# Performance work log

Hardware: AMD Instinct MI355X
Metric: run time of the kernel (lower is better)

Reference implementation:

```python
import jax, jax.numpy as jnp
import numpy as np

B, C, H, W = 2, 64, 128, 128
HEADS = 8
HID = C  # hidden_size = dim in MHSA.__init__
EPS = 1e-12  # F.normalize default eps


def setup_inputs() -> dict:
    key = jax.random.key(0)
    ks = jax.random.split(key, 9)
    s = 0.05
    return {
        "x": jax.random.normal(ks[0], (B, C, H, W), jnp.float32),
        "W1": jax.random.normal(ks[1], (C, HID), jnp.float32) * s,
        "b1": jax.random.normal(ks[2], (C, HID), jnp.float32) * s,
        "W2": jax.random.normal(ks[3], (C, HID, HID), jnp.float32) * s,
        "b2": jax.random.normal(ks[4], (C, HID), jnp.float32) * s,
        "W3": jax.random.normal(ks[5], (C, HID, 3), jnp.float32) * s,
        "b3": jax.random.normal(ks[6], (C, 3), jnp.float32) * s,
        "temperature": jnp.ones((HEADS, 1, 1), jnp.float32),
        "Wout": jax.random.normal(ks[7], (C, C), jnp.float32) * s,  # [out, in] 1x1 conv
        "bout": jax.random.normal(ks[8], (C,), jnp.float32) * s,
    }


def reference(x, W1, b1, W2, b2, W3, b3, temperature, Wout, bout):
    b, c, h, w = x.shape
    # KAN QKV projection: per-channel tiny MLPs, batched over the channel axis.
    xt = jnp.transpose(x, (0, 2, 3, 1)).reshape(-1, c)          # [N, C]
    h1 = jax.nn.relu(xt[:, :, None] * W1[None] + b1[None])      # [N, C, HID]
    h2 = jax.nn.relu(jnp.einsum('nch,chk->nck', h1, W2) + b2[None])  # [N, C, HID]
    o = jnp.einsum('nch,cho->nco', h2, W3) + b3[None]           # [N, C, 3]
    # torch.cat of per-channel 3-col outputs along dim=1 == reshape [N, C*3]
    qkv = o.reshape(b, h, w, c * 3)
    qkv = jnp.transpose(qkv, (0, 3, 1, 2))                      # [b, 3c, h, w]
    q, k, v = jnp.split(qkv, 3, axis=1)                         # each [b, c, h, w]

    def to_heads(t):
        return t.reshape(b, HEADS, c // HEADS, h * w)

    q, k, v = to_heads(q), to_heads(k), to_heads(v)
    # L2-normalize along the spatial (last) axis, torch F.normalize semantics
    q = q / jnp.maximum(jnp.linalg.norm(q, axis=-1, keepdims=True), EPS)
    k = k / jnp.maximum(jnp.linalg.norm(k, axis=-1, keepdims=True), EPS)
    # Channel attention: [b, head, c_h, c_h]
    attn = jnp.einsum('bhcn,bhdn->bhcd', q, k) * temperature[None]
    attn = jax.nn.softmax(attn, axis=-1)
    out = jnp.einsum('bhcd,bhdn->bhcn', attn, v)                # [b, head, c_h, hw]
    out = out.reshape(b, c, h, w)
    # 1x1 conv projection
    out = jnp.einsum('bchw,oc->bohw', out, Wout) + bout[None, :, None, None]
    return out
```

## Files before the change

### kernel.cpp

```cpp
#include <hip/hip_runtime.h>
#include <hip/hip_bf16.h>
#include <math.h>

#define HW 16384
#define NCH 64

#define NG   2048
#define X0   (-8.0f)
#define INVDX 128.0f
#define DX   0.0078125f
#define PSTR (64*2048)

typedef __attribute__((ext_vector_type(8))) short s16x8;
typedef __attribute__((ext_vector_type(4))) short s16x4;
typedef __attribute__((ext_vector_type(2))) float f32x2;
typedef __attribute__((ext_vector_type(4))) float f32x4;
typedef __attribute__((ext_vector_type(8))) float f32x8;
typedef __attribute__((ext_vector_type(2))) __bf16 bf16x2;
typedef __attribute__((ext_vector_type(8))) __bf16 bf16x8;
typedef __attribute__((ext_vector_type(4))) unsigned u32x4;
typedef __attribute__((ext_vector_type(2))) unsigned u32x2;

__device__ __forceinline__ short bf16b(float f) {
    union { __hip_bfloat16 h; short s; } u;
    u.h = __float2bfloat16(f);
    return u.s;
}
__device__ __forceinline__ float bf2f(unsigned short us) {
    union { unsigned u; float f; } x;
    x.u = ((unsigned)us) << 16;
    return x.f;
}
__device__ __forceinline__ s16x8 cvt8(f32x8 v) {
    return __builtin_bit_cast(s16x8, __builtin_convertvector(v, bf16x8));
}
__device__ __forceinline__ unsigned pk_h1(f32x2 xw, f32x2 w, f32x2 b, f32x2 z2) {
    const f32x2 h = __builtin_elementwise_max(__builtin_elementwise_fma(xw, w, b), z2);
    return __builtin_bit_cast(unsigned, __builtin_convertvector(h, bf16x2));
}
__device__ __forceinline__ unsigned pk_relu_cvt(f32x2 v, f32x2 z2) {
    const f32x2 g = __builtin_elementwise_max(v, z2);
    return __builtin_bit_cast(unsigned, __builtin_convertvector(g, bf16x2));
}

#if __has_builtin(__builtin_amdgcn_mfma_f32_16x16x16bf16_1k)
#define HAVE_MFMA16 1
#else
#define HAVE_MFMA16 0
#endif

__global__ __launch_bounds__(64, 4) void kan_grid_mfma(
    const float* __restrict__ W1,
    const float* __restrict__ b1,
    const float* __restrict__ W2,
    const float* __restrict__ b2,
    const float* __restrict__ W3,
    const float* __restrict__ b3,
    float* __restrict__ table)
{
    const int c     = blockIdx.x & 63;
    const int chunk = blockIdx.x >> 6;
    const int lane  = threadIdx.x;
    const int l15   = lane & 15;
    const int grp   = lane >> 4;

    __shared__ float W2s[4096];
    __shared__ float W1s[64], B1s[64], B2s[64];
    {
        const float4* src = (const float4*)(W2 + c * 4096);
        float4* dst = (float4*)W2s;
        for (int i = lane; i < 1024; i += 64) dst[i] = src[i];
        W1s[lane] = W1[c*64 + lane];
        B1s[lane] = b1[c*64 + lane];
        B2s[lane] = b2[c*64 + lane];
    }
    __syncthreads();

    const float* W3c = W3 + c * 192;

    s16x8 a1[4][2];
#pragma unroll
    for (int m = 0; m < 4; ++m)
#pragma unroll
        for (int s = 0; s < 2; ++s) {
            f32x8 w;
#pragma unroll
            for (int jj = 0; jj < 8; ++jj)
                w[jj] = W2s[(s*32 + grp*8 + jj)*64 + m*16 + l15];
            a1[m][s] = cvt8(w);
        }

#if HAVE_MFMA16
    s16x4 a2[4];
#pragma unroll
    for (int m = 0; m < 4; ++m) {
        s16x4 f;
#pragma unroll
        for (int jj = 0; jj < 4; ++jj) {
            const int k = m*16 + grp*4 + jj;
            f[jj] = (l15 < 3) ? bf16b(W3c[k*3 + l15]) : (short)0;
        }
        a2[m] = f;
    }
    f32x4 b3r;
#pragma unroll
    for (int r = 0; r < 4; ++r) {
        const int row = grp*4 + r;
        b3r[r] = (row < 3) ? b3[c*3 + row] : 0.f;
    }
#else
    const float b3v0 = b3[c*3+0], b3v1 = b3[c*3+1], b3v2 = b3[c*3+2];
#endif

    float* Tq = table + c*NG;
    const char* b2base = (const char*)B2s;
    const f32x2 z2 = {0.f, 0.f};

    for (int t = 0; t < 16; ++t) {
        int z;
        asm volatile("v_mov_b32 %0, 0" : "=v"(z));

        const int pt = chunk*256 + t*16 + l15;
        const float xv = X0 + (float)pt * DX;
        const f32x2 xw = {xv, xv};

        s16x8 bf[2];
#pragma unroll
        for (int s = 0; s < 2; ++s) {
            const f32x4 w1lo = *(const f32x4*)&W1s[z + s*32 + grp*8];
            const f32x4 w1hi = *(const f32x4*)&W1s[z + s*32 + grp*8 + 4];
            const f32x4 b1lo = *(const f32x4*)&B1s[z + s*32 + grp*8];
            const f32x4 b1hi = *(const f32x4*)&B1s[z + s*32 + grp*8 + 4];
            u32x4 p;
            p[0] = pk_h1(xw, (f32x2){w1lo[0], w1lo[1]}, (f32x2){b1lo[0], b1lo[1]}, z2);
            p[1] = pk_h1(xw, (f32x2){w1lo[2], w1lo[3]}, (f32x2){b1lo[2], b1lo[3]}, z2);
            p[2] = pk_h1(xw, (f32x2){w1hi[0], w1hi[1]}, (f32x2){b1hi[0], b1hi[1]}, z2);
            p[3] = pk_h1(xw, (f32x2){w1hi[2], w1hi[3]}, (f32x2){b1hi[2], b1hi[3]}, z2);
            bf[s] = __builtin_bit_cast(s16x8, p);
        }

        f32x4 acc[4];
#pragma unroll
        for (int m = 0; m < 4; ++m) {
            acc[m] = *(const f32x4*)(b2base + (m*64 + grp*16 + z));
            acc[m] = __builtin_amdgcn_mfma_f32_16x16x32_bf16(a1[m][0], bf[0], acc[m], 0, 0, 0);
            acc[m] = __builtin_amdgcn_mfma_f32_16x16x32_bf16(a1[m][1], bf[1], acc[m], 0, 0, 0);
        }

#if HAVE_MFMA16
        s16x4 bb[4];
#pragma unroll
        for (int m = 0; m < 4; ++m) {
            u32x2 pv;
            pv[0] = pk_relu_cvt((f32x2){acc[m][0], acc[m][1]}, z2);
            pv[1] = pk_relu_cvt((f32x2){acc[m][2], acc[m][3]}, z2);
            bb[m] = __builtin_bit_cast(s16x4, pv);
        }
        f32x4 acc2a = b3r;
        f32x4 acc2b = {0.f, 0.f, 0.f, 0.f};
        acc2a = __builtin_amdgcn_mfma_f32_16x16x16bf16_1k(a2[0], bb[0], acc2a, 0, 0, 0);
        acc2b = __builtin_amdgcn_mfma_f32_16x16x16bf16_1k(a2[1], bb[1], acc2b, 0, 0, 0);
        acc2a = __builtin_amdgcn_mfma_f32_16x16x16bf16_1k(a2[2], bb[2], acc2a, 0, 0, 0);
        acc2b = __builtin_amdgcn_mfma_f32_16x16x16bf16_1k(a2[3], bb[3], acc2b, 0, 0, 0);
        if (grp == 0) {
            Tq[pt]          = acc2a[0] + acc2b[0];
            Tq[PSTR + pt]   = acc2a[1] + acc2b[1];
            Tq[2*PSTR + pt] = acc2a[2] + acc2b[2];
        }
#else
        float po0 = 0.f, po1 = 0.f, po2 = 0.f;
#pragma unroll
        for (int m = 0; m < 4; ++m)
#pragma unroll
            for (int r = 0; r < 4; ++r) {
                const float g = fmaxf(acc[m][r], 0.f);
                const int k = m*16 + grp*4 + r;
                po0 = fmaf(g, W3c[k*3+0], po0);
                po1 = fmaf(g, W3c[k*3+1], po1);
                po2 = fmaf(g, W3c[k*3+2], po2);
            }
        po0 += __shfl_xor(po0, 16, 64); po0 += __shfl_xor(po0, 32, 64);
        po1 += __shfl_xor(po1, 16, 64); po1 += __shfl_xor(po1, 32, 64);
        po2 += __shfl_xor(po2, 16, 64); po2 += __shfl_xor(po2, 32, 64);
        if (grp == 0) {
            Tq[pt]          = po0 + b3v0;
            Tq[PSTR + pt]   = po1 + b3v1;
            Tq[2*PSTR + pt] = po2 + b3v2;
        }
#endif
    }
}

__global__ __launch_bounds__(512) void gram_kernel(
    const float* __restrict__ x, const float* __restrict__ table,
    float* __restrict__ dpart)
{
    const int bhd = blockIdx.x >> 4;
    const int spl = blockIdx.x & 15;
    const int b = bhd >> 3, hd = bhd & 7;
    const int tid = threadIdx.x;
    const int w   = tid >> 6;
    const int l   = tid & 63;
    const int grp = l >> 4;
    const int i16 = l & 15;
    const int ch  = i16 & 7;
    const int usek = i16 >> 3;

    __shared__ unsigned short T[2][8][NG];

    for (int e = tid; e < 8192; e += 512) {
        const int map = e >> 12;
        const int rem = e & 4095;
        const int c8  = rem >> 9;
        const int g   = rem & 511;
        const int gm  = map*64 + hd*8 + c8;
        const int cc  = gm / 3;
        const int jj  = gm % 3;
        const float4 v = ((const float4*)(table + jj*PSTR + cc*NG))[g];
        u32x2 pk;
        pk[0] = ((unsigned)(unsigned short)bf16b(v.x)) | (((unsigned)(unsigned short)bf16b(v.y)) << 16);
        pk[1] = ((unsigned)(unsigned short)bf16b(v.z)) | (((unsigned)(unsigned short)bf16b(v.w)) << 16);
        *(u32x2*)&T[map][c8][g*4] = pk;
    }
    __syncthreads();

    const unsigned short* Tc = T[usek][ch];
    const int gm = usek*64 + hd*8 + ch;
    const int cx = gm / 3;
    const float* xp = x + (b*NCH + cx)*HW + spl*1024 + grp*8;

    f32x4 gacc = {0.f, 0.f, 0.f, 0.f};
#pragma unroll
    for (int s = 0; s < 4; ++s) {
        const int slab = w*4 + s;
        const float* xs = xp + slab*32;
        const f32x4 xlo = *(const f32x4*)xs;
        const f32x4 xhi = *(const f32x4*)(xs + 4);
        f32x8 vals;
#pragma unroll
        for (int e = 0; e < 8; ++e) {
            const float xv = (e < 4) ? xlo[e] : xhi[e-4];
            const float u = (xv - X0) * INVDX;
            int idx = (int)u;
            idx = min(max(idx, 0), NG - 2);
            const float fr = u - (float)idx;
            const float t0 = bf2f(Tc[idx]);
            const float t1 = bf2f(Tc[idx+1]);
            vals[e] = fmaf(fr, t1 - t0, t0);
        }
        const s16x8 frag = cvt8(vals);
        gacc = __builtin_amdgcn_mfma_f32_16x16x32_bf16(frag, frag, gacc, 0, 0, 0);
    }

    __syncthreads();
    float* red = (float*)&T[0][0][0];
#pragma unroll
    for (int r = 0; r < 4; ++r)
        red[w*256 + (grp*4 + r)*16 + i16] = gacc[r];
    __syncthreads();

    if (tid < 256) {
        const int row = tid >> 4, col = tid & 15;
        float g = 0.f;
#pragma unroll
        for (int ww = 0; ww < 8; ++ww) g += red[ww*256 + tid];
        int p = -1;
        if (row < 8 && col >= 8)      p = row*8 + (col - 8);
        else if (row == col && row < 8) p = 64 + row;
        else if (row == col)            p = 72 + (row - 8);
        if (p >= 0) dpart[(bhd*16 + spl)*80 + p] = g;
    }
}

__global__ __launch_bounds__(256) void v_eval(
    const float* __restrict__ x, const float* __restrict__ table,
    unsigned short* __restrict__ vbuf)
{
    const int m     = blockIdx.x >> 3;
    const int chunk = blockIdx.x & 7;
    const int t     = threadIdx.x;
    const int gm    = 128 + m;
    const int cx    = gm / 3;
    const int jj    = gm % 3;

    __shared__ float Lv[NG];
    const float4* Tv = (const float4*)(table + jj*PSTR + cx*NG);
    for (int i = t; i < NG/4; i += 256) ((float4*)Lv)[i] = Tv[i];
    __syncthreads();

    const int pxbase = chunk * 4096;
    const int b  = pxbase >> 14;
    const int hw = pxbase & 16383;
    const float* xr = x + (b*NCH + cx)*HW + hw;
    unsigned short* vr = vbuf + (b*NCH + m)*HW + hw;

    for (int i = 0; i < 8; ++i) {
        const int off = i*512 + t*2;
        const float2 xv = *(const float2*)(xr + off);
        float o[2];
#pragma unroll
        for (int e = 0; e < 2; ++e) {
            const float u = ((e ? xv.y : xv.x) - X0) * INVDX;
            int idx = (int)u;
            idx = min(max(idx, 0), NG - 2);
            const float fr = u - (float)idx;
            const float v0 = Lv[idx], v1 = Lv[idx+1];
            o[e] = fmaf(fr, v1 - v0, v0);
        }
        ushort2 vs;
        vs.x = (unsigned short)bf16b(o[0]);
        vs.y = (unsigned short)bf16b(o[1]);
        *(ushort2*)(vr + off) = vs;
    }
}

__global__ __launch_bounds__(256) void out_kernel(
    const unsigned short* __restrict__ vbuf, const float* __restrict__ dpart,
    const float* __restrict__ temp, const float* __restrict__ Wout,
    const float* __restrict__ bout, float* __restrict__ out)
{
    const int b    = blockIdx.x >> 8;
    const int qtr  = (blockIdx.x >> 6) & 3;
    const int tile = blockIdx.x & 63;
    const int n = tile * 256 + threadIdx.x;
    const int t = threadIdx.x;

    __shared__ float D[8][80];
    __shared__ float attnS[8][8][8];
    __shared__ float4 AtS[64][4];

    for (int idx = t; idx < 640; idx += 256) {
        const int g = idx / 80, p = idx % 80;
        float s = 0.f;
        for (int spl = 0; spl < 16; ++spl)
            s += dpart[((b*8 + g)*16 + spl)*80 + p];
        D[g][p] = s;
    }
    __syncthreads();

    if (t < 64) {
        const int hd = t >> 3, i = t & 7;
        const float invq = 1.f / fmaxf(sqrtf(D[hd][64+i]), 1e-12f);
        const float T = temp[hd];
        float l[8];
        float m = -1e30f;
#pragma unroll
        for (int j = 0; j < 8; ++j) {
            const float invk = 1.f / fmaxf(sqrtf(D[hd][72+j]), 1e-12f);
            l[j] = D[hd][i*8+j] * invq * invk * T;
            m = fmaxf(m, l[j]);
        }
        float s = 0.f;
#pragma unroll
        for (int j = 0; j < 8; ++j) { l[j] = expf(l[j] - m); s += l[j]; }
        const float inv = 1.f / s;
#pragma unroll
        for (int j = 0; j < 8; ++j) attnS[hd][i][j] = l[j] * inv;
    }
    __syncthreads();

    {
        const int cv = t & 63, oq = t >> 6;
        const int hd = cv >> 3, jj = cv & 7;
        float res[4];
#pragma unroll
        for (int oo = 0; oo < 4; ++oo) {
            const int o = qtr*16 + oq*4 + oo;
            float s = 0.f;
#pragma unroll
            for (int i = 0; i < 8; ++i)
                s = fmaf(Wout[o*64 + hd*8 + i], attnS[hd][i][jj], s);
            res[oo] = s;
        }
        AtS[cv][oq] = make_float4(res[0], res[1], res[2], res[3]);
    }
    __syncthreads();

    float acc[16];
#pragma unroll
    for (int o = 0; o < 16; ++o) acc[o] = 0.f;

    const unsigned short* vbase = vbuf + (b*NCH)*HW + n;
    for (int cv = 0; cv < 64; ++cv) {
        const float vv = bf2f(vbase[cv*HW]);
#pragma unroll
        for (int o4 = 0; o4 < 4; ++o4) {
            const float4 w = AtS[cv][o4];
            acc[4*o4+0] = fmaf(w.x, vv, acc[4*o4+0]);
            acc[4*o4+1] = fmaf(w.y, vv, acc[4*o4+1]);
            acc[4*o4+2] = fmaf(w.z, vv, acc[4*o4+2]);
            acc[4*o4+3] = fmaf(w.w, vv, acc[4*o4+3]);
        }
    }
#pragma unroll
    for (int o = 0; o < 16; ++o) {
        const int oc = qtr*16 + o;
        out[(b*NCH + oc)*HW + n] = acc[o] + bout[oc];
    }
}

extern "C" void kernel_launch(void* const* d_in, const int* in_sizes, int n_in,
                              void* d_out, int out_size, void* d_ws, size_t ws_size,
                              hipStream_t stream) {
    const float* x    = (const float*)d_in[0];
    const float* W1   = (const float*)d_in[1];
    const float* b1   = (const float*)d_in[2];
    const float* W2   = (const float*)d_in[3];
    const float* b2   = (const float*)d_in[4];
    const float* W3   = (const float*)d_in[5];
    const float* b3   = (const float*)d_in[6];
    const float* temp = (const float*)d_in[7];
    const float* Wout = (const float*)d_in[8];
    const float* bout = (const float*)d_in[9];
    float* out = (float*)d_out;

    float* ws = (float*)d_ws;
    float* table = ws;
    float* dpart = ws + 393216;
    unsigned short* vbuf = (unsigned short*)(ws + 393216 + 20480);

    kan_grid_mfma<<<512, 64, 0, stream>>>(W1, b1, W2, b2, W3, b3, table);
    gram_kernel<<<256, 512, 0, stream>>>(x, table, dpart);
    v_eval<<<512, 256, 0, stream>>>(x, table, vbuf);
    out_kernel<<<512, 256, 0, stream>>>(vbuf, dpart, temp, Wout, bout, out);
}
```

Baseline: 52.78 us.

## Fuse four kernels into one cooperative kernel with grid-wide syncs

Merges the table-build, gram, v-eval and output kernels into a single cooperative launch of 256 blocks of 512 threads, separated by grid.sync(). The work split per block changes: the table phase runs on only 64 blocks, and v-eval and output cover larger slices per block. The aim is to remove three kernel-launch gaps and inter-kernel drain/fill. In exchange, grid syncs add their own cost, and the table phase leaves most of the grid idle with larger per-block work.

```diff
diff --git a/kernel.cpp b/kernel.cpp
--- a/kernel.cpp
+++ b/kernel.cpp
@@ -1,6 +1,9 @@
 #include <hip/hip_runtime.h>
+#include <hip/hip_cooperative_groups.h>
 #include <hip/hip_bf16.h>
 #include <math.h>
+
+namespace cg = cooperative_groups;
 
 #define HW 16384
 #define NCH 64
@@ -49,353 +52,356 @@
 #define HAVE_MFMA16 0
 #endif
 
-__global__ __launch_bounds__(64, 4) void kan_grid_mfma(
-    const float* __restrict__ W1,
-    const float* __restrict__ b1,
-    const float* __restrict__ W2,
-    const float* __restrict__ b2,
-    const float* __restrict__ W3,
-    const float* __restrict__ b3,
-    float* __restrict__ table)
-{
-    const int c     = blockIdx.x & 63;
-    const int chunk = blockIdx.x >> 6;
-    const int lane  = threadIdx.x;
-    const int l15   = lane & 15;
-    const int grp   = lane >> 4;
-
-    __shared__ float W2s[4096];
-    __shared__ float W1s[64], B1s[64], B2s[64];
-    {
-        const float4* src = (const float4*)(W2 + c * 4096);
-        float4* dst = (float4*)W2s;
-        for (int i = lane; i < 1024; i += 64) dst[i] = src[i];
-        W1s[lane] = W1[c*64 + lane];
-        B1s[lane] = b1[c*64 + lane];
-        B2s[lane] = b2[c*64 + lane];
-    }
-    __syncthreads();
-
-    const float* W3c = W3 + c * 192;
-
-    s16x8 a1[4][2];
-#pragma unroll
-    for (int m = 0; m < 4; ++m)
-#pragma unroll
-        for (int s = 0; s < 2; ++s) {
-            f32x8 w;
-#pragma unroll
-            for (int jj = 0; jj < 8; ++jj)
-                w[jj] = W2s[(s*32 + grp*8 + jj)*64 + m*16 + l15];
-            a1[m][s] = cvt8(w);
-        }
-
-#if HAVE_MFMA16
-    s16x4 a2[4];
-#pragma unroll
-    for (int m = 0; m < 4; ++m) {
-        s16x4 f;
-#pragma unroll
-        for (int jj = 0; jj < 4; ++jj) {
-            const int k = m*16 + grp*4 + jj;
-            f[jj] = (l15 < 3) ? bf16b(W3c[k*3 + l15]) : (short)0;
-        }
-        a2[m] = f;
-    }
-    f32x4 b3r;
-#pragma unroll
-    for (int r = 0; r < 4; ++r) {
-        const int row = grp*4 + r;
-        b3r[r] = (row < 3) ? b3[c*3 + row] : 0.f;
-    }
-#else
-    const float b3v0 = b3[c*3+0], b3v1 = b3[c*3+1], b3v2 = b3[c*3+2];
-#endif
-
-    float* Tq = table + c*NG;
-    const char* b2base = (const char*)B2s;
-    const f32x2 z2 = {0.f, 0.f};
-
-    for (int t = 0; t < 16; ++t) {
-        int z;
-        asm volatile("v_mov_b32 %0, 0" : "=v"(z));
-
-        const int pt = chunk*256 + t*16 + l15;
-        const float xv = X0 + (float)pt * DX;
-        const f32x2 xw = {xv, xv};
-
-        s16x8 bf[2];
-#pragma unroll
-        for (int s = 0; s < 2; ++s) {
-            const f32x4 w1lo = *(const f32x4*)&W1s[z + s*32 + grp*8];
-            const f32x4 w1hi = *(const f32x4*)&W1s[z + s*32 + grp*8 + 4];
-            const f32x4 b1lo = *(const f32x4*)&B1s[z + s*32 + grp*8];
-            const f32x4 b1hi = *(const f32x4*)&B1s[z + s*32 + grp*8 + 4];
-            u32x4 p;
-            p[0] = pk_h1(xw, (f32x2){w1lo[0], w1lo[1]}, (f32x2){b1lo[0], b1lo[1]}, z2);
-            p[1] = pk_h1(xw, (f32x2){w1lo[2], w1lo[3]}, (f32x2){b1lo[2], b1lo[3]}, z2);
-            p[2] = pk_h1(xw, (f32x2){w1hi[0], w1hi[1]}, (f32x2){b1hi[0], b1hi[1]}, z2);
-            p[3] = pk_h1(xw, (f32x2){w1hi[2], w1hi[3]}, (f32x2){b1hi[2], b1hi[3]}, z2);
-            bf[s] = __builtin_bit_cast(s16x8, p);
-        }
-
-        f32x4 acc[4];
-#pragma unroll
-        for (int m = 0; m < 4; ++m) {
-            acc[m] = *(const f32x4*)(b2base + (m*64 + grp*16 + z));
-            acc[m] = __builtin_amdgcn_mfma_f32_16x16x32_bf16(a1[m][0], bf[0], acc[m], 0, 0, 0);
-            acc[m] = __builtin_amdgcn_mfma_f32_16x16x32_bf16(a1[m][1], bf[1], acc[m], 0, 0, 0);
-        }
-
-#if HAVE_MFMA16
-        s16x4 bb[4];
-#pragma unroll
-        for (int m = 0; m < 4; ++m) {
-            u32x2 pv;
-            pv[0] = pk_relu_cvt((f32x2){acc[m][0], acc[m][1]}, z2);
-            pv[1] = pk_relu_cvt((f32x2){acc[m][2], acc[m][3]}, z2);
-            bb[m] = __builtin_bit_cast(s16x4, pv);
-        }
-        f32x4 acc2a = b3r;
-        f32x4 acc2b = {0.f, 0.f, 0.f, 0.f};
-        acc2a = __builtin_amdgcn_mfma_f32_16x16x16bf16_1k(a2[0], bb[0], acc2a, 0, 0, 0);
-        acc2b = __builtin_amdgcn_mfma_f32_16x16x16bf16_1k(a2[1], bb[1], acc2b, 0, 0, 0);
-        acc2a = __builtin_amdgcn_mfma_f32_16x16x16bf16_1k(a2[2], bb[2], acc2a, 0, 0, 0);
-        acc2b = __builtin_amdgcn_mfma_f32_16x16x16bf16_1k(a2[3], bb[3], acc2b, 0, 0, 0);
-        if (grp == 0) {
-            Tq[pt]          = acc2a[0] + acc2b[0];
-            Tq[PSTR + pt]   = acc2a[1] + acc2b[1];
-            Tq[2*PSTR + pt] = acc2a[2] + acc2b[2];
-        }
-#else
-        float po0 = 0.f, po1 = 0.f, po2 = 0.f;
-#pragma unroll
-        for (int m = 0; m < 4; ++m)
-#pragma unroll
-            for (int r = 0; r < 4; ++r) {
-                const float g = fmaxf(acc[m][r], 0.f);
-                const int k = m*16 + grp*4 + r;
-                po0 = fmaf(g, W3c[k*3+0], po0);
-                po1 = fmaf(g, W3c[k*3+1], po1);
-                po2 = fmaf(g, W3c[k*3+2], po2);
-            }
-        po0 += __shfl_xor(po0, 16, 64); po0 += __shfl_xor(po0, 32, 64);
-        po1 += __shfl_xor(po1, 16, 64); po1 += __shfl_xor(po1, 32, 64);
-        po2 += __shfl_xor(po2, 16, 64); po2 += __shfl_xor(po2, 32, 64);
-        if (grp == 0) {
-            Tq[pt]          = po0 + b3v0;
-            Tq[PSTR + pt]   = po1 + b3v1;
-            Tq[2*PSTR + pt] = po2 + b3v2;
-        }
-#endif
-    }
-}
-
-__global__ __launch_bounds__(512) void gram_kernel(
-    const float* __restrict__ x, const float* __restrict__ table,
-    float* __restrict__ dpart)
-{
-    const int bhd = blockIdx.x >> 4;
-    const int spl = blockIdx.x & 15;
-    const int b = bhd >> 3, hd = bhd & 7;
-    const int tid = threadIdx.x;
-    const int w   = tid >> 6;
-    const int l   = tid & 63;
-    const int grp = l >> 4;
-    const int i16 = l & 15;
-    const int ch  = i16 & 7;
-    const int usek = i16 >> 3;
-
-    __shared__ unsigned short T[2][8][NG];
-
-    for (int e = tid; e < 8192; e += 512) {
-        const int map = e >> 12;
-        const int rem = e & 4095;
-        const int c8  = rem >> 9;
-        const int g   = rem & 511;
-        const int gm  = map*64 + hd*8 + c8;
-        const int cc  = gm / 3;
-        const int jj  = gm % 3;
-        const float4 v = ((const float4*)(table + jj*PSTR + cc*NG))[g];
-        u32x2 pk;
-        pk[0] = ((unsigned)(unsigned short)bf16b(v.x)) | (((unsigned)(unsigned short)bf16b(v.y)) << 16);
-        pk[1] = ((unsigned)(unsigned short)bf16b(v.z)) | (((unsigned)(unsigned short)bf16b(v.w)) << 16);
-        *(u32x2*)&T[map][c8][g*4] = pk;
-    }
-    __syncthreads();
-
-    const unsigned short* Tc = T[usek][ch];
-    const int gm = usek*64 + hd*8 + ch;
-    const int cx = gm / 3;
-    const float* xp = x + (b*NCH + cx)*HW + spl*1024 + grp*8;
-
-    f32x4 gacc = {0.f, 0.f, 0.f, 0.f};
-#pragma unroll
-    for (int s = 0; s < 4; ++s) {
-        const int slab = w*4 + s;
-        const float* xs = xp + slab*32;
-        const f32x4 xlo = *(const f32x4*)xs;
-        const f32x4 xhi = *(const f32x4*)(xs + 4);
-        f32x8 vals;
-#pragma unroll
-        for (int e = 0; e < 8; ++e) {
-            const float xv = (e < 4) ? xlo[e] : xhi[e-4];
-            const float u = (xv - X0) * INVDX;
-            int idx = (int)u;
-            idx = min(max(idx, 0), NG - 2);
-            const float fr = u - (float)idx;
-            const float t0 = bf2f(Tc[idx]);
-            const float t1 = bf2f(Tc[idx+1]);
-            vals[e] = fmaf(fr, t1 - t0, t0);
-        }
-        const s16x8 frag = cvt8(vals);
-        gacc = __builtin_amdgcn_mfma_f32_16x16x32_bf16(frag, frag, gacc, 0, 0, 0);
-    }
-
-    __syncthreads();
-    float* red = (float*)&T[0][0][0];
-#pragma unroll
-    for (int r = 0; r < 4; ++r)
-        red[w*256 + (grp*4 + r)*16 + i16] = gacc[r];
-    __syncthreads();
-
-    if (tid < 256) {
-        const int row = tid >> 4, col = tid & 15;
-        float g = 0.f;
-#pragma unroll
-        for (int ww = 0; ww < 8; ++ww) g += red[ww*256 + tid];
-        int p = -1;
-        if (row < 8 && col >= 8)      p = row*8 + (col - 8);
-        else if (row == col && row < 8) p = 64 + row;
-        else if (row == col)            p = 72 + (row - 8);
-        if (p >= 0) dpart[(bhd*16 + spl)*80 + p] = g;
-    }
-}
-
-__global__ __launch_bounds__(256) void v_eval(
-    const float* __restrict__ x, const float* __restrict__ table,
+__global__ __launch_bounds__(512, 2) void fused_mhsa(
+    const float* __restrict__ x,
+    const float* __restrict__ W1, const float* __restrict__ b1,
+    const float* __restrict__ W2, const float* __restrict__ b2,
+    const float* __restrict__ W3, const float* __restrict__ b3,
+    const float* __restrict__ temp, const float* __restrict__ Wout,
+    const float* __restrict__ bout, float* __restrict__ out,
+    float* __restrict__ table, float* __restrict__ dpart,
     unsigned short* __restrict__ vbuf)
 {
-    const int m     = blockIdx.x >> 3;
-    const int chunk = blockIdx.x & 7;
-    const int t     = threadIdx.x;
-    const int gm    = 128 + m;
-    const int cx    = gm / 3;
-    const int jj    = gm % 3;
-
-    __shared__ float Lv[NG];
-    const float4* Tv = (const float4*)(table + jj*PSTR + cx*NG);
-    for (int i = t; i < NG/4; i += 256) ((float4*)Lv)[i] = Tv[i];
-    __syncthreads();
-
-    const int pxbase = chunk * 4096;
-    const int b  = pxbase >> 14;
-    const int hw = pxbase & 16383;
-    const float* xr = x + (b*NCH + cx)*HW + hw;
-    unsigned short* vr = vbuf + (b*NCH + m)*HW + hw;
-
-    for (int i = 0; i < 8; ++i) {
-        const int off = i*512 + t*2;
-        const float2 xv = *(const float2*)(xr + off);
-        float o[2];
-#pragma unroll
-        for (int e = 0; e < 2; ++e) {
-            const float u = ((e ? xv.y : xv.x) - X0) * INVDX;
-            int idx = (int)u;
-            idx = min(max(idx, 0), NG - 2);
-            const float fr = u - (float)idx;
-            const float v0 = Lv[idx], v1 = Lv[idx+1];
-            o[e] = fmaf(fr, v1 - v0, v0);
-        }
-        ushort2 vs;
-        vs.x = (unsigned short)bf16b(o[0]);
-        vs.y = (unsigned short)bf16b(o[1]);
-        *(ushort2*)(vr + off) = vs;
+    __shared__ __align__(16) unsigned char LB[65536];
+    cg::grid_group grid = cg::this_grid();
+    const int bi  = blockIdx.x;
+    const int tid = threadIdx.x;
+
+    if (bi < 64) {
+        const int c = bi;
+        float* W2s = (float*)LB;
+        float* W1s = (float*)(LB + 16384);
+        float* B1s = (float*)(LB + 16640);
+        float* B2s = (float*)(LB + 16896);
+        {
+            const float4* src = (const float4*)(W2 + c * 4096);
+            float4* dst = (float4*)W2s;
+            for (int i = tid; i < 1024; i += 512) dst[i] = src[i];
+            if (tid < 64) {
+                W1s[tid] = W1[c*64 + tid];
+                B1s[tid] = b1[c*64 + tid];
+                B2s[tid] = b2[c*64 + tid];
+            }
+        }
+        __syncthreads();
+
+        const int lane  = tid & 63;
+        const int chunk = tid >> 6;
+        const int l15   = lane & 15;
+        const int grp   = lane >> 4;
+        const float* W3c = W3 + c * 192;
+
+        s16x8 a1[4][2];
+#pragma unroll
+        for (int m = 0; m < 4; ++m)
+#pragma unroll
+            for (int s = 0; s < 2; ++s) {
+                f32x8 w;
+#pragma unroll
+                for (int jj = 0; jj < 8; ++jj)
+                    w[jj] = W2s[(s*32 + grp*8 + jj)*64 + m*16 + l15];
+                a1[m][s] = cvt8(w);
+            }
+
+#if HAVE_MFMA16
+        s16x4 a2[4];
+#pragma unroll
+        for (int m = 0; m < 4; ++m) {
+            s16x4 f;
+#pragma unroll
+            for (int jj = 0; jj < 4; ++jj) {
+                const int k = m*16 + grp*4 + jj;
+                f[jj] = (l15 < 3) ? bf16b(W3c[k*3 + l15]) : (short)0;
+            }
+            a2[m] = f;
+        }
+        f32x4 b3r;
+#pragma unroll
+        for (int r = 0; r < 4; ++r) {
+            const int row = grp*4 + r;
+            b3r[r] = (row < 3) ? b3[c*3 + row] : 0.f;
+        }
+#else
+        const float b3v0 = b3[c*3+0], b3v1 = b3[c*3+1], b3v2 = b3[c*3+2];
+#endif
+
+        float* Tq = table + c*NG;
+        const char* b2base = (const char*)B2s;
+        const f32x2 z2 = {0.f, 0.f};
+
+        for (int t = 0; t < 16; ++t) {
+            int z;
+            asm volatile("v_mov_b32 %0, 0" : "=v"(z));
+
+            const int pt = chunk*256 + t*16 + l15;
+            const float xv = X0 + (float)pt * DX;
+            const f32x2 xw = {xv, xv};
+
+            s16x8 bf[2];
+#pragma unroll
+            for (int s = 0; s < 2; ++s) {
+                const f32x4 w1lo = *(const f32x4*)&W1s[z + s*32 + grp*8];
+                const f32x4 w1hi = *(const f32x4*)&W1s[z + s*32 + grp*8 + 4];
+                const f32x4 b1lo = *(const f32x4*)&B1s[z + s*32 + grp*8];
+                const f32x4 b1hi = *(const f32x4*)&B1s[z + s*32 + grp*8 + 4];
+                u32x4 p;
+                p[0] = pk_h1(xw, (f32x2){w1lo[0], w1lo[1]}, (f32x2){b1lo[0], b1lo[1]}, z2);
+                p[1] = pk_h1(xw, (f32x2){w1lo[2], w1lo[3]}, (f32x2){b1lo[2], b1lo[3]}, z2);
+                p[2] = pk_h1(xw, (f32x2){w1hi[0], w1hi[1]}, (f32x2){b1hi[0], b1hi[1]}, z2);
+                p[3] = pk_h1(xw, (f32x2){w1hi[2], w1hi[3]}, (f32x2){b1hi[2], b1hi[3]}, z2);
+                bf[s] = __builtin_bit_cast(s16x8, p);
+            }
+
+            f32x4 acc[4];
+#pragma unroll
+            for (int m = 0; m < 4; ++m) {
+                acc[m] = *(const f32x4*)(b2base + (m*64 + grp*16 + z));
+                acc[m] = __builtin_amdgcn_mfma_f32_16x16x32_bf16(a1[m][0], bf[0], acc[m], 0, 0, 0);
+                acc[m] = __builtin_amdgcn_mfma_f32_16x16x32_bf16(a1[m][1], bf[1], acc[m], 0, 0, 0);
+            }
+
+#if HAVE_MFMA16
+            s16x4 bb[4];
+#pragma unroll
+            for (int m = 0; m < 4; ++m) {
+                u32x2 pv;
+                pv[0] = pk_relu_cvt((f32x2){acc[m][0], acc[m][1]}, z2);
+                pv[1] = pk_relu_cvt((f32x2){acc[m][2], acc[m][3]}, z2);
+                bb[m] = __builtin_bit_cast(s16x4, pv);
+            }
+            f32x4 acc2a = b3r;
+            f32x4 acc2b = {0.f, 0.f, 0.f, 0.f};
+            acc2a = __builtin_amdgcn_mfma_f32_16x16x16bf16_1k(a2[0], bb[0], acc2a, 0, 0, 0);
+            acc2b = __builtin_amdgcn_mfma_f32_16x16x16bf16_1k(a2[1], bb[1], acc2b, 0, 0, 0);
+            acc2a = __builtin_amdgcn_mfma_f32_16x16x16bf16_1k(a2[2], bb[2], acc2a, 0, 0, 0);
+            acc2b = __builtin_amdgcn_mfma_f32_16x16x16bf16_1k(a2[3], bb[3], acc2b, 0, 0, 0);
+            if (grp == 0) {
+                Tq[pt]          = acc2a[0] + acc2b[0];
+                Tq[PSTR + pt]   = acc2a[1] + acc2b[1];
+                Tq[2*PSTR + pt] = acc2a[2] + acc2b[2];
+            }
+#else
+            float po0 = 0.f, po1 = 0.f, po2 = 0.f;
+#pragma unroll
+            for (int m = 0; m < 4; ++m)
+#pragma unroll
+                for (int r = 0; r < 4; ++r) {
+                    const float g = fmaxf(acc[m][r], 0.f);
+                    const int k = m*16 + grp*4 + r;
+                    po0 = fmaf(g, W3c[k*3+0], po0);
+                    po1 = fmaf(g, W3c[k*3+1], po1);
+                    po2 = fmaf(g, W3c[k*3+2], po2);
+                }
+            po0 += __shfl_xor(po0, 16, 64); po0 += __shfl_xor(po0, 32, 64);
+            po1 += __shfl_xor(po1, 16, 64); po1 += __shfl_xor(po1, 32, 64);
+            po2 += __shfl_xor(po2, 16, 64); po2 += __shfl_xor(po2, 32, 64);
+            if (grp == 0) {
+                Tq[pt]          = po0 + b3v0;
+                Tq[PSTR + pt]   = po1 + b3v1;
+                Tq[2*PSTR + pt] = po2 + b3v2;
+            }
+#endif
+        }
     }
-}
-
-__global__ __launch_bounds__(256) void out_kernel(
-    const unsigned short* __restrict__ vbuf, const float* __restrict__ dpart,
-    const float* __restrict__ temp, const float* __restrict__ Wout,
-    const float* __restrict__ bout, float* __restrict__ out)
-{
-    const int b    = blockIdx.x >> 8;
-    const int qtr  = (blockIdx.x >> 6) & 3;
-    const int tile = blockIdx.x & 63;
-    const int n = tile * 256 + threadIdx.x;
-    const int t = threadIdx.x;
-
-    __shared__ float D[8][80];
-    __shared__ float attnS[8][8][8];
-    __shared__ float4 AtS[64][4];
-
-    for (int idx = t; idx < 640; idx += 256) {
-        const int g = idx / 80, p = idx % 80;
-        float s = 0.f;
-        for (int spl = 0; spl < 16; ++spl)
-            s += dpart[((b*8 + g)*16 + spl)*80 + p];
-        D[g][p] = s;
+
+    grid.sync();
+
+    {
+        const int bhd = bi >> 4;
+        const int spl = bi & 15;
+        const int b = bhd >> 3, hd = bhd & 7;
+        const int w   = tid >> 6;
+        const int l   = tid & 63;
+        const int grp = l >> 4;
+        const int i16 = l & 15;
+        const int ch  = i16 & 7;
+        const int usek = i16 >> 3;
+
+        unsigned short* T = (unsigned short*)LB;
+
+        __syncthreads();
+        for (int e = tid; e < 8192; e += 512) {
+            const int map = e >> 12;
+            const int rem = e & 4095;
+            const int c8  = rem >> 9;
+            const int g   = rem & 511;
+            const int gm  = map*64 + hd*8 + c8;
+            const int cc  = gm / 3;
+            const int jj  = gm % 3;
+            const float4 v = ((const float4*)(table + jj*PSTR + cc*NG))[g];
+            u32x2 pk;
+            pk[0] = ((unsigned)(unsigned short)bf16b(v.x)) | (((unsigned)(unsigned short)bf16b(v.y)) << 16);
+            pk[1] = ((unsigned)(unsigned short)bf16b(v.z)) | (((unsigned)(unsigned short)bf16b(v.w)) << 16);
+            *(u32x2*)&T[(map*8 + c8)*NG + g*4] = pk;
+        }
+        __syncthreads();
+
+        const unsigned short* Tc = &T[(usek*8 + ch)*NG];
+        const int gm = usek*64 + hd*8 + ch;
+        const int cx = gm / 3;
+        const float* xp = x + (b*NCH + cx)*HW + spl*1024 + grp*8;
+
+        f32x4 gacc = {0.f, 0.f, 0.f, 0.f};
+#pragma unroll
+        for (int s = 0; s < 4; ++s) {
+            const int slab = w*4 + s;
+            const float* xs = xp + slab*32;
+            const f32x4 xlo = *(const f32x4*)xs;
+            const f32x4 xhi = *(const f32x4*)(xs + 4);
+            f32x8 vals;
+#pragma unroll
+            for (int e = 0; e < 8; ++e) {
+                const float xv = (e < 4) ? xlo[e] : xhi[e-4];
+                const float u = (xv - X0) * INVDX;
+                int idx = (int)u;
+                idx = min(max(idx, 0), NG - 2);
+                const float fr = u - (float)idx;
+                const float t0 = bf2f(Tc[idx]);
+                const float t1 = bf2f(Tc[idx+1]);
+                vals[e] = fmaf(fr, t1 - t0, t0);
+            }
+            const s16x8 frag = cvt8(vals);
+            gacc = __builtin_amdgcn_mfma_f32_16x16x32_bf16(frag, frag, gacc, 0, 0, 0);
+        }
+
+        __syncthreads();
+        float* red = (float*)LB;
+#pragma unroll
+        for (int r = 0; r < 4; ++r)
+            red[w*256 + (grp*4 + r)*16 + i16] = gacc[r];
+        __syncthreads();
+
+        if (tid < 256) {
+            const int row = tid >> 4, col = tid & 15;
+            float g = 0.f;
+#pragma unroll
+            for (int ww = 0; ww < 8; ++ww) g += red[ww*256 + tid];
+            int p = -1;
+            if (row < 8 && col >= 8)        p = row*8 + (col - 8);
+            else if (row == col && row < 8) p = 64 + row;
+            else if (row == col)            p = 72 + (row - 8);
+            if (p >= 0) dpart[(bhd*16 + spl)*80 + p] = g;
+        }
+        __syncthreads();
     }
-    __syncthreads();
-
-    if (t < 64) {
-        const int hd = t >> 3, i = t & 7;
-        const float invq = 1.f / fmaxf(sqrtf(D[hd][64+i]), 1e-12f);
-        const float T = temp[hd];
-        float l[8];
-        float m = -1e30f;
-#pragma unroll
-        for (int j = 0; j < 8; ++j) {
-            const float invk = 1.f / fmaxf(sqrtf(D[hd][72+j]), 1e-12f);
-            l[j] = D[hd][i*8+j] * invq * invk * T;
-            m = fmaxf(m, l[j]);
-        }
-        float s = 0.f;
-#pragma unroll
-        for (int j = 0; j < 8; ++j) { l[j] = expf(l[j] - m); s += l[j]; }
-        const float inv = 1.f / s;
-#pragma unroll
-        for (int j = 0; j < 8; ++j) attnS[hd][i][j] = l[j] * inv;
+
+    {
+        const int m    = bi >> 2;
+        const int half = bi & 3;
+        const int gm   = 128 + m;
+        const int cx   = gm / 3;
+        const int jj   = gm % 3;
+
+        float* Lv = (float*)LB;
+        ((float4*)Lv)[tid] = ((const float4*)(table + jj*PSTR + cx*NG))[tid];
+        __syncthreads();
+
+        const int pbase = half * 8192;
+        const int b  = pbase >> 14;
+        const int hw = pbase & 16383;
+        const float* xr = x + (b*NCH + cx)*HW + hw;
+        unsigned short* vr = vbuf + (b*NCH + m)*HW + hw;
+
+        for (int i = 0; i < 8; ++i) {
+            const int off = i*1024 + tid*2;
+            const float2 xv = *(const float2*)(xr + off);
+            float o[2];
+#pragma unroll
+            for (int e = 0; e < 2; ++e) {
+                const float u = ((e ? xv.y : xv.x) - X0) * INVDX;
+                int idx = (int)u;
+                idx = min(max(idx, 0), NG - 2);
+                const float fr = u - (float)idx;
+                const float v0 = Lv[idx], v1 = Lv[idx+1];
+                o[e] = fmaf(fr, v1 - v0, v0);
+            }
+            ushort2 vs;
+            vs.x = (unsigned short)bf16b(o[0]);
+            vs.y = (unsigned short)bf16b(o[1]);
+            *(ushort2*)(vr + off) = vs;
+        }
     }
-    __syncthreads();
+
+    grid.sync();
 
     {
-        const int cv = t & 63, oq = t >> 6;
-        const int hd = cv >> 3, jj = cv & 7;
-        float res[4];
-#pragma unroll
-        for (int oo = 0; oo < 4; ++oo) {
-            const int o = qtr*16 + oq*4 + oo;
+        const int b   = bi >> 7;
+        const int qtr = (bi >> 5) & 3;
+        const int tp  = bi & 31;
+        const int n   = tp*512 + tid;
+
+        float*  D     = (float*)LB;
+        float*  attnS = (float*)(LB + 2560);
+        float4* AtS   = (float4*)(LB + 4608);
+
+        for (int idx = tid; idx < 640; idx += 512) {
+            const int g = idx / 80, p = idx % 80;
             float s = 0.f;
-#pragma unroll
-            for (int i = 0; i < 8; ++i)
-                s = fmaf(Wout[o*64 + hd*8 + i], attnS[hd][i][jj], s);
-            res[oo] = s;
-        }
-        AtS[cv][oq] = make_float4(res[0], res[1], res[2], res[3]);
-    }
-    __syncthreads();
-
-    float acc[16];
-#pragma unroll
-    for (int o = 0; o < 16; ++o) acc[o] = 0.f;
-
-    const unsigned short* vbase = vbuf + (b*NCH)*HW + n;
-    for (int cv = 0; cv < 64; ++cv) {
-        const float vv = bf2f(vbase[cv*HW]);
-#pragma unroll
-        for (int o4 = 0; o4 < 4; ++o4) {
-            const float4 w = AtS[cv][o4];
-            acc[4*o4+0] = fmaf(w.x, vv, acc[4*o4+0]);
-            acc[4*o4+1] = fmaf(w.y, vv, acc[4*o4+1]);
-            acc[4*o4+2] = fmaf(w.z, vv, acc[4*o4+2]);
-            acc[4*o4+3] = fmaf(w.w, vv, acc[4*o4+3]);
-        }
-    }
-#pragma unroll
-    for (int o = 0; o < 16; ++o) {
-        const int oc = qtr*16 + o;
-        out[(b*NCH + oc)*HW + n] = acc[o] + bout[oc];
+            for (int spl = 0; spl < 16; ++spl)
+                s += dpart[((b*8 + g)*16 + spl)*80 + p];
+            D[g*80 + p] = s;
+        }
+        __syncthreads();
+
+        if (tid < 64) {
+            const int hd = tid >> 3, i = tid & 7;
+            const float invq = 1.f / fmaxf(sqrtf(D[hd*80 + 64 + i]), 1e-12f);
+            const float T = temp[hd];
+            float l[8];
+            float m = -1e30f;
+#pragma unroll
+            for (int j = 0; j < 8; ++j) {
+                const float invk = 1.f / fmaxf(sqrtf(D[hd*80 + 72 + j]), 1e-12f);
+                l[j] = D[hd*80 + i*8 + j] * invq * invk * T;
+                m = fmaxf(m, l[j]);
+            }
+            float s = 0.f;
+#pragma unroll
+            for (int j = 0; j < 8; ++j) { l[j] = expf(l[j] - m); s += l[j]; }
+            const float inv = 1.f / s;
+#pragma unroll
+            for (int j = 0; j < 8; ++j) attnS[(hd*8 + i)*8 + j] = l[j] * inv;
+        }
+        __syncthreads();
+
+        if (tid < 256) {
+            const int cv = tid & 63, oq = tid >> 6;
+            const int hd = cv >> 3, jj = cv & 7;
+            float res[4];
+#pragma unroll
+            for (int oo = 0; oo < 4; ++oo) {
+                const int o = qtr*16 + oq*4 + oo;
+                float s = 0.f;
+#pragma unroll
+                for (int i = 0; i < 8; ++i)
+                    s = fmaf(Wout[o*64 + hd*8 + i], attnS[(hd*8 + i)*8 + jj], s);
+                res[oo] = s;
+            }
+            AtS[cv*4 + oq] = make_float4(res[0], res[1], res[2], res[3]);
+        }
+        __syncthreads();
+
+        float acc[16];
+#pragma unroll
+        for (int o = 0; o < 16; ++o) acc[o] = 0.f;
+
+        const unsigned short* vbase = vbuf + (b*NCH)*HW + n;
+        for (int cv = 0; cv < 64; ++cv) {
+            const float vv = bf2f(vbase[cv*HW]);
+#pragma unroll
+            for (int o4 = 0; o4 < 4; ++o4) {
+                const float4 w = AtS[cv*4 + o4];
+                acc[4*o4+0] = fmaf(w.x, vv, acc[4*o4+0]);
+                acc[4*o4+1] = fmaf(w.y, vv, acc[4*o4+1]);
+                acc[4*o4+2] = fmaf(w.z, vv, acc[4*o4+2]);
+                acc[4*o4+3] = fmaf(w.w, vv, acc[4*o4+3]);
+            }
+        }
+#pragma unroll
+        for (int o = 0; o < 16; ++o) {
+            const int oc = qtr*16 + o;
+            out[(b*NCH + oc)*HW + n] = acc[o] + bout[oc];
+        }
     }
 }
 
@@ -419,8 +425,11 @@
     float* dpart = ws + 393216;
     unsigned short* vbuf = (unsigned short*)(ws + 393216 + 20480);
 
-    kan_grid_mfma<<<512, 64, 0, stream>>>(W1, b1, W2, b2, W3, b3, table);
-    gram_kernel<<<256, 512, 0, stream>>>(x, table, dpart);
-    v_eval<<<512, 256, 0, stream>>>(x, table, vbuf);
-    out_kernel<<<512, 256, 0, stream>>>(vbuf, dpart, temp, Wout, bout, out);
-}
+    void* args[] = {
+        (void*)&x, (void*)&W1, (void*)&b1, (void*)&W2, (void*)&b2,
+        (void*)&W3, (void*)&b3, (void*)&temp, (void*)&Wout, (void*)&bout,
+        (void*)&out, (void*)&table, (void*)&dpart, (void*)&vbuf
+    };
+    hipLaunchCooperativeKernel((const void*)fused_mhsa, dim3(256), dim3(512),
+                               args, 0, stream);
+}
```

Measured after the change: 109.9 us. +108.3%, slower.

## Double grid sizes across all kernels and reduce gram partials with atomics

Applied to the files above, without the earlier changes.

Every kernel now launches twice as many blocks, each doing half the work: half the grid points in kan_grid_mfma, half the pixels per gram/v_eval block, and 8 output channels per out_kernel block instead of 16. The gram partial sums are accumulated into a zeroed global buffer with atomicAdd, so out_kernel reads the final values directly instead of summing 16 partials. The aim is better CU occupancy on the 256-CU device and a shorter reduction in out_kernel. The cost is an extra memset launch, atomic contention, non-deterministic summation order, and each out_kernel block reading vbuf for fewer outputs, so vbuf is re-read twice as often.

```diff
diff --git a/kernel.cpp b/kernel.cpp
--- a/kernel.cpp
+++ b/kernel.cpp
@@ -116,11 +116,11 @@
     const char* b2base = (const char*)B2s;
     const f32x2 z2 = {0.f, 0.f};
 
-    for (int t = 0; t < 16; ++t) {
+    for (int t = 0; t < 8; ++t) {
         int z;
         asm volatile("v_mov_b32 %0, 0" : "=v"(z));
 
-        const int pt = chunk*256 + t*16 + l15;
+        const int pt = chunk*128 + t*16 + l15;
         const float xv = X0 + (float)pt * DX;
         const f32x2 xw = {xv, xv};
 
@@ -193,10 +193,10 @@
 
 __global__ __launch_bounds__(512) void gram_kernel(
     const float* __restrict__ x, const float* __restrict__ table,
-    float* __restrict__ dpart)
+    float* __restrict__ Dglob)
 {
-    const int bhd = blockIdx.x >> 4;
-    const int spl = blockIdx.x & 15;
+    const int bhd = blockIdx.x >> 5;
+    const int spl = blockIdx.x & 31;
     const int b = bhd >> 3, hd = bhd & 7;
     const int tid = threadIdx.x;
     const int w   = tid >> 6;
@@ -227,12 +227,12 @@
     const unsigned short* Tc = T[usek][ch];
     const int gm = usek*64 + hd*8 + ch;
     const int cx = gm / 3;
-    const float* xp = x + (b*NCH + cx)*HW + spl*1024 + grp*8;
+    const float* xp = x + (b*NCH + cx)*HW + spl*512 + grp*8;
 
     f32x4 gacc = {0.f, 0.f, 0.f, 0.f};
 #pragma unroll
-    for (int s = 0; s < 4; ++s) {
-        const int slab = w*4 + s;
+    for (int s = 0; s < 2; ++s) {
+        const int slab = w*2 + s;
         const float* xs = xp + slab*32;
         const f32x4 xlo = *(const f32x4*)xs;
         const f32x4 xhi = *(const f32x4*)(xs + 4);
@@ -265,10 +265,10 @@
 #pragma unroll
         for (int ww = 0; ww < 8; ++ww) g += red[ww*256 + tid];
         int p = -1;
-        if (row < 8 && col >= 8)      p = row*8 + (col - 8);
+        if (row < 8 && col >= 8)        p = row*8 + (col - 8);
         else if (row == col && row < 8) p = 64 + row;
         else if (row == col)            p = 72 + (row - 8);
-        if (p >= 0) dpart[(bhd*16 + spl)*80 + p] = g;
+        if (p >= 0) atomicAdd(&Dglob[bhd*80 + p], g);
     }
 }
 
@@ -276,8 +276,8 @@
     const float* __restrict__ x, const float* __restrict__ table,
     unsigned short* __restrict__ vbuf)
 {
-    const int m     = blockIdx.x >> 3;
-    const int chunk = blockIdx.x & 7;
+    const int m     = blockIdx.x >> 4;
+    const int chunk = blockIdx.x & 15;
     const int t     = threadIdx.x;
     const int gm    = 128 + m;
     const int cx    = gm / 3;
@@ -288,13 +288,13 @@
     for (int i = t; i < NG/4; i += 256) ((float4*)Lv)[i] = Tv[i];
     __syncthreads();
 
-    const int pxbase = chunk * 4096;
+    const int pxbase = chunk * 2048;
     const int b  = pxbase >> 14;
     const int hw = pxbase & 16383;
     const float* xr = x + (b*NCH + cx)*HW + hw;
     unsigned short* vr = vbuf + (b*NCH + m)*HW + hw;
 
-    for (int i = 0; i < 8; ++i) {
+    for (int i = 0; i < 4; ++i) {
         const int off = i*512 + t*2;
         const float2 xv = *(const float2*)(xr + off);
         float o[2];
@@ -315,27 +315,22 @@
 }
 
 __global__ __launch_bounds__(256) void out_kernel(
-    const unsigned short* __restrict__ vbuf, const float* __restrict__ dpart,
+    const unsigned short* __restrict__ vbuf, const float* __restrict__ Dglob,
     const float* __restrict__ temp, const float* __restrict__ Wout,
     const float* __restrict__ bout, float* __restrict__ out)
 {
-    const int b    = blockIdx.x >> 8;
-    const int qtr  = (blockIdx.x >> 6) & 3;
+    const int b    = blockIdx.x >> 9;
+    const int og   = (blockIdx.x >> 6) & 7;
     const int tile = blockIdx.x & 63;
     const int n = tile * 256 + threadIdx.x;
     const int t = threadIdx.x;
 
     __shared__ float D[8][80];
     __shared__ float attnS[8][8][8];
-    __shared__ float4 AtS[64][4];
-
-    for (int idx = t; idx < 640; idx += 256) {
-        const int g = idx / 80, p = idx % 80;
-        float s = 0.f;
-        for (int spl = 0; spl < 16; ++spl)
-            s += dpart[((b*8 + g)*16 + spl)*80 + p];
-        D[g][p] = s;
-    }
+    __shared__ float2 AtS[64][4];
+
+    for (int idx = t; idx < 640; idx += 256)
+        ((float*)D)[idx] = Dglob[b*640 + idx];
     __syncthreads();
 
     if (t < 64) {
@@ -359,42 +354,47 @@
     }
     __syncthreads();
 
-    {
+    if (t < 128) {
         const int cv = t & 63, oq = t >> 6;
         const int hd = cv >> 3, jj = cv & 7;
         float res[4];
 #pragma unroll
         for (int oo = 0; oo < 4; ++oo) {
-            const int o = qtr*16 + oq*4 + oo;
+            const int o = og*8 + oq*4 + oo;
             float s = 0.f;
 #pragma unroll
             for (int i = 0; i < 8; ++i)
                 s = fmaf(Wout[o*64 + hd*8 + i], attnS[hd][i][jj], s);
             res[oo] = s;
         }
-        AtS[cv][oq] = make_float4(res[0], res[1], res[2], res[3]);
-    }
-    __syncthreads();
-
-    float acc[16];
-#pragma unroll
-    for (int o = 0; o < 16; ++o) acc[o] = 0.f;
+        AtS[cv][oq*2 + 0] = make_float2(res[0], res[1]);
+        AtS[cv][oq*2 + 1] = make_float2(res[2], res[3]);
+    }
+    __syncthreads();
+
+    float acc[8];
+#pragma unroll
+    for (int o = 0; o < 8; ++o) acc[o] = 0.f;
 
     const unsigned short* vbase = vbuf + (b*NCH)*HW + n;
     for (int cv = 0; cv < 64; ++cv) {
         const float vv = bf2f(vbase[cv*HW]);
-#pragma unroll
-        for (int o4 = 0; o4 < 4; ++o4) {
-            const float4 w = AtS[cv][o4];
-            acc[4*o4+0] = fmaf(w.x, vv, acc[4*o4+0]);
-            acc[4*o4+1] = fmaf(w.y, vv, acc[4*o4+1]);
-            acc[4*o4+2] = fmaf(w.z, vv, acc[4*o4+2]);
-            acc[4*o4+3] = fmaf(w.w, vv, acc[4*o4+3]);
-        }
-    }
-#pragma unroll
-    for (int o = 0; o < 16; ++o) {
-        const int oc = qtr*16 + o;
+        const float2 w0 = AtS[cv][0];
+        const float2 w1 = AtS[cv][1];
+        const float2 w2 = AtS[cv][2];
+        const float2 w3 = AtS[cv][3];
+        acc[0] = fmaf(w0.x, vv, acc[0]);
+        acc[1] = fmaf(w0.y, vv, acc[1]);
+        acc[2] = fmaf(w1.x, vv, acc[2]);
+        acc[3] = fmaf(w1.y, vv, acc[3]);
+        acc[4] = fmaf(w2.x, vv, acc[4]);
+        acc[5] = fmaf(w2.y, vv, acc[5]);
+        acc[6] = fmaf(w3.x, vv, acc[6]);
+        acc[7] = fmaf(w3.y, vv, acc[7]);
+    }
+#pragma unroll
+    for (int o = 0; o < 8; ++o) {
+        const int oc = og*8 + o;
         out[(b*NCH + oc)*HW + n] = acc[o] + bout[oc];
     }
 }
@@ -416,11 +416,12 @@
 
     float* ws = (float*)d_ws;
     float* table = ws;
-    float* dpart = ws + 393216;
-    unsigned short* vbuf = (unsigned short*)(ws + 393216 + 20480);
-
-    kan_grid_mfma<<<512, 64, 0, stream>>>(W1, b1, W2, b2, W3, b3, table);
-    gram_kernel<<<256, 512, 0, stream>>>(x, table, dpart);
-    v_eval<<<512, 256, 0, stream>>>(x, table, vbuf);
-    out_kernel<<<512, 256, 0, stream>>>(vbuf, dpart, temp, Wout, bout, out);
-}
+    float* Dglob = ws + 393216;
+    unsigned short* vbuf = (unsigned short*)(ws + 393216 + 1280);
+
+    hipMemsetAsync(Dglob, 0, 1280 * sizeof(float), stream);
+    kan_grid_mfma<<<1024, 64, 0, stream>>>(W1, b1, W2, b2, W3, b3, table);
+    gram_kernel<<<512, 512, 0, stream>>>(x, table, Dglob);
+    v_eval<<<1024, 256, 0, stream>>>(x, table, vbuf);
+    out_kernel<<<1024, 256, 0, stream>>>(vbuf, Dglob, temp, Wout, bout, out);
+}
```

Result: no change. 51.98 us (-1.5%).
